# Optimization experiments

Measured on AMD Instinct MI355X. Metric: run time of the kernel, lower is better.

Reference implementation:

```python
import jax, jax.numpy as jnp
import numpy as np

EMBED_DIM = 1024
BOTTLENECK = 48          # adapter_hidden_dim (adapter_rank=0)
ADAPTER_WIDTH = 1        # multivector channels
MV_DIM = 16              # Cl(1,3) multivector dimension
N_GRADES = 5             # grades of sizes 1,4,6,4,1
LN_EPS = 1e-5

# grade projection mask [5,16]: grade0=idx0, grade1=1:5, grade2=5:11, grade3=11:15, grade4=15
_gm = np.zeros((N_GRADES, MV_DIM), dtype=np.float32)
_gm[0, 0] = 1.0
_gm[1, 1:5] = 1.0
_gm[2, 5:11] = 1.0
_gm[3, 11:15] = 1.0
_gm[4, 15] = 1.0
GRADE_MASK = jnp.asarray(_gm)


def setup_inputs() -> dict:
    key = jax.random.key(0)
    ks = jax.random.split(key, 8)
    B, N, D, R, W = 128, 256, EMBED_DIM, BOTTLENECK, ADAPTER_WIDTH
    x = jax.random.normal(ks[0], (B, N, D), dtype=jnp.float32)
    gamma = jnp.ones((D,), dtype=jnp.float32)
    beta = jnp.zeros((D,), dtype=jnp.float32)
    w_down = jax.random.normal(ks[1], (R, D), dtype=jnp.float32) / np.sqrt(D)
    w_to_mv = jax.random.normal(ks[2], (W * MV_DIM, R), dtype=jnp.float32) / np.sqrt(R)
    w_equi = jax.random.normal(ks[3], (W, W, N_GRADES), dtype=jnp.float32)
    b_equi = jnp.zeros((W,), dtype=jnp.float32)
    w_from_mv = jax.random.normal(ks[4], (R, W * MV_DIM), dtype=jnp.float32) / np.sqrt(W * MV_DIM)
    w_up = jax.random.normal(ks[5], (D, R), dtype=jnp.float32) / np.sqrt(R)
    scale = jnp.float32(0.001)
    return {"x": x, "gamma": gamma, "beta": beta, "w_down": w_down,
            "w_to_mv": w_to_mv, "w_equi": w_equi, "b_equi": b_equi,
            "w_from_mv": w_from_mv, "w_up": w_up, "scale": scale}


def reference(x, gamma, beta, w_down, w_to_mv, w_equi, b_equi, w_from_mv, w_up, scale):
    B, N, D = x.shape
    # LayerNorm
    mu = jnp.mean(x, axis=-1, keepdims=True)
    var = jnp.mean(jnp.square(x - mu), axis=-1, keepdims=True)
    h = (x - mu) * jax.lax.rsqrt(var + LN_EPS) * gamma + beta
    # down + GELU (exact, matching torch F.gelu default)
    h = jax.nn.gelu(jnp.einsum('bnd,rd->bnr', h, w_down), approximate=False)
    # to multivectors [B,N,C,16]
    mv = jnp.einsum('bnr,mr->bnm', h, w_to_mv).reshape(B, N, -1, MV_DIM)
    # EquiLinear: per-grade channel mixing + scalar bias
    mv = jnp.einsum('oik,kj,bnij->bnoj', w_equi, GRADE_MASK, mv)
    mv = mv.at[..., 0].add(b_equi)
    # from multivectors + GELU
    h = jax.nn.gelu(jnp.einsum('bnm,rm->bnr', mv.reshape(B, N, -1), w_from_mv),
                    approximate=False)
    # up (dropout p=0 is identity) and scaled residual
    h = jnp.einsum('bnr,dr->bnd', h, w_up)
    return x + scale * h
```

## Files before the change

kernel.cpp:

```cpp
#include <hip/hip_runtime.h>
#include <hip/hip_bf16.h>


typedef __attribute__((ext_vector_type(8))) short short8;
typedef __attribute__((ext_vector_type(4))) short short4b;
typedef __attribute__((ext_vector_type(4))) float float4a;

#define NTOK 32768
#define D 1024

__device__ __forceinline__ short f2bf(float x) {
    unsigned u = __float_as_uint(x);
    unsigned r = u + 0x7FFFu + ((u >> 16) & 1u);
    return (short)(r >> 16);
}
__device__ __forceinline__ float bf2f(short s) {
    return __uint_as_float(((unsigned)(unsigned short)s) << 16);
}
__device__ __forceinline__ float gelu_exact(float v) {
    return 0.5f * v * (1.0f + erff(v * 0.70710678118654752f));
}

__global__ void prep_weights(const float* __restrict__ wdn_f, const float* __restrict__ wup_f,
                             const float* __restrict__ gamma, const float* __restrict__ beta,
                             short* __restrict__ wdn_b, short* __restrict__ wup_b,
                             float* __restrict__ c12) {
    int blk = blockIdx.x;
    int tid = threadIdx.x;
    if (blk < 192) {
        int o = blk * 256 + tid;
        int j = o & 7, lane = (o >> 3) & 63, kt = (o >> 9) & 31, cb = o >> 14;
        int r = cb * 16 + (lane & 15);
        int d = kt * 32 + (lane >> 4) * 8 + j;
        wdn_b[o] = f2bf(wdn_f[r * 1024 + d] * gamma[d]);
    } else if (blk < 448) {
        int o2 = (blk - 192) * 256 + tid;
        int j = o2 & 7, lane = (o2 >> 3) & 63, kt = (o2 >> 9) & 1, cb = o2 >> 10;
        int dcol = cb * 16 + (lane & 15);
        int r = kt * 32 + (lane >> 4) * 8 + j;
        wup_b[o2] = (r < 48) ? f2bf(wup_f[dcol * 48 + r]) : (short)0;
    } else {
        int r = blk - 448;
        float a = 0.f, b = 0.f;
#pragma unroll
        for (int i = 0; i < 4; ++i) {
            int d = tid + 256 * i;
            float wv = wdn_f[r * 1024 + d];
            a = fmaf(wv, gamma[d], a);
            b = fmaf(wv, beta[d], b);
        }
#pragma unroll
        for (int off = 32; off; off >>= 1) {
            a += __shfl_xor(a, off);
            b += __shfl_xor(b, off);
        }
        __shared__ float red[8];
        int lane = tid & 63, w = tid >> 6;
        if (lane == 0) { red[w] = a; red[4 + w] = b; }
        __syncthreads();
        if (tid == 0) {
            c12[r]      = red[0] + red[1] + red[2] + red[3];
            c12[48 + r] = red[4] + red[5] + red[6] + red[7];
        }
    }
}

__launch_bounds__(256, 4)
__global__ void adapter_main(const float* __restrict__ x, const float* __restrict__ w_to_mv,
                             const float* __restrict__ w_equi, const float* __restrict__ b_equi,
                             const float* __restrict__ w_from_mv, const float* __restrict__ scale_p,
                             const short* __restrict__ wdn_b, const short* __restrict__ wup_b,
                             const float* __restrict__ c12, float* __restrict__ out) {
    __shared__ __align__(16) short xsh[16][1032];
    __shared__ __align__(16) float scratch[1568];
    short* zbuf = (short*)scratch;

    const int tid  = threadIdx.x;
    const int lane = tid & 63;
    const int w    = tid >> 6;
    const int q    = lane >> 4;
    const int m    = lane & 15;
    const long token0 = (long)blockIdx.x * 16;

    {
        const float4* xr = (const float4*)(x + token0 * D);
        float4 v[16];
#pragma unroll
        for (int t = 0; t < 4; ++t)
#pragma unroll
            for (int i = 0; i < 4; ++i)
                v[t * 4 + i] = xr[(w * 4 + t) * 256 + lane + 64 * i];

#pragma unroll
        for (int t = 0; t < 4; ++t) {
            int tok = w * 4 + t;
            float s1 = 0.f, s2 = 0.f;
#pragma unroll
            for (int i = 0; i < 4; ++i) {
                float4 vv = v[t * 4 + i];
                s1 += vv.x + vv.y + vv.z + vv.w;
                s2 += vv.x * vv.x + vv.y * vv.y + vv.z * vv.z + vv.w * vv.w;
            }
#pragma unroll
            for (int off = 32; off; off >>= 1) {
                s1 += __shfl_xor(s1, off);
                s2 += __shfl_xor(s2, off);
            }
            float mu  = s1 * (1.0f / 1024.0f);
            float var = fmaf(-mu, mu, s2 * (1.0f / 1024.0f));
            float rs  = rsqrtf(var + 1e-5f);
#pragma unroll
            for (int i = 0; i < 4; ++i) {
                int d0 = 4 * lane + 256 * i;
                float4 vv = v[t * 4 + i];
                short4b xs = {f2bf(vv.x), f2bf(vv.y), f2bf(vv.z), f2bf(vv.w)};
                *(short4b*)&xsh[tok][d0] = xs;
            }
            if (lane == 0) {
                scratch[1536 + tok] = rs;
                scratch[1552 + tok] = -mu * rs;
            }
        }
    }
    __syncthreads();

#pragma unroll
    for (int rep = 0; rep < 2; ++rep) {
        int jid = w + rep * 4;
        if (jid < 6) {
            int cb = jid % 3, kh = jid / 3;
            float4a acc = {0.f, 0.f, 0.f, 0.f};
            const short* bptr = wdn_b + ((cb * 32 + kh * 16) * 64 + lane) * 8;
            const short* aptr = &xsh[m][kh * 512 + q * 8];
#pragma unroll
            for (int kt = 0; kt < 16; ++kt) {
                short8 a = *(const short8*)(aptr + kt * 32);
                short8 b = *(const short8*)(bptr + kt * 512);
                acc = __builtin_amdgcn_mfma_f32_16x16x32_bf16(a, b, acc, 0, 0, 0);
            }
#pragma unroll
            for (int i = 0; i < 4; ++i)
                scratch[kh * 768 + (q * 4 + i) * 48 + cb * 16 + m] = acc[i];
        }
    }
    __syncthreads();

#pragma unroll
    for (int k = 0; k < 3; ++k) {
        int it = tid + k * 256;
        int tt = it / 48, r = it - tt * 48;
        float s = scratch[tt * 48 + r] + scratch[768 + tt * 48 + r];
        float y = fmaf(scratch[1536 + tt], s, fmaf(scratch[1552 + tt], c12[r], c12[48 + r]));
        scratch[tt * 48 + r] = gelu_exact(y);
    }
    __syncthreads();
    {
        int tt = tid >> 4, j = tid & 15;
        float acc = 0.f;
#pragma unroll 8
        for (int r = 0; r < 48; ++r) acc = fmaf(w_to_mv[j * 48 + r], scratch[tt * 48 + r], acc);
        int g = (j == 0) ? 0 : (j < 5) ? 1 : (j < 11) ? 2 : (j < 15) ? 3 : 4;
        acc *= w_equi[g];
        if (j == 0) acc += b_equi[0];
        scratch[768 + tt * 16 + j] = acc;
    }
    __syncthreads();
#pragma unroll
    for (int k = 0; k < 3; ++k) {
        int it = tid + k * 256;
        int tt = it / 48, r = it - tt * 48;
        float acc = 0.f;
#pragma unroll
        for (int j = 0; j < 16; ++j) acc = fmaf(w_from_mv[r * 16 + j], scratch[768 + tt * 16 + j], acc);
        float z = gelu_exact(acc);
        int kt = r >> 5, qq = (r >> 3) & 3, jj = r & 7;
        zbuf[kt * 512 + (qq * 16 + tt) * 8 + jj] = f2bf(z);
    }
    zbuf[768 + tid] = 0;
    __syncthreads();

    const float scale = scale_p[0];
    short8 a0 = *(const short8*)&zbuf[lane * 8];
    short8 a1 = *(const short8*)&zbuf[512 + lane * 8];
    long rowbase = (token0 + q * 4) * D;
#pragma unroll 4
    for (int cc = 0; cc < 16; ++cc) {
        int cb = w * 16 + cc;
        short8 b0 = *(const short8*)(wup_b + (cb * 2 + 0) * 512 + lane * 8);
        short8 b1 = *(const short8*)(wup_b + (cb * 2 + 1) * 512 + lane * 8);
        float4a acc = {0.f, 0.f, 0.f, 0.f};
        acc = __builtin_amdgcn_mfma_f32_16x16x32_bf16(a0, b0, acc, 0, 0, 0);
        acc = __builtin_amdgcn_mfma_f32_16x16x32_bf16(a1, b1, acc, 0, 0, 0);
        int d = cb * 16 + m;
#pragma unroll
        for (int i = 0; i < 4; ++i) {
            int tok = q * 4 + i;
            float xv = bf2f(xsh[tok][d]);
            out[rowbase + (long)i * D + d] = fmaf(scale, acc[i], xv);
        }
    }
}

extern "C" void kernel_launch(void* const* d_in, const int* in_sizes, int n_in,
                              void* d_out, int out_size, void* d_ws, size_t ws_size,
                              hipStream_t stream) {
    const float* x         = (const float*)d_in[0];
    const float* gamma     = (const float*)d_in[1];
    const float* beta      = (const float*)d_in[2];
    const float* w_down    = (const float*)d_in[3];
    const float* w_to_mv   = (const float*)d_in[4];
    const float* w_equi    = (const float*)d_in[5];
    const float* b_equi    = (const float*)d_in[6];
    const float* w_from_mv = (const float*)d_in[7];
    const float* w_up      = (const float*)d_in[8];
    const float* scale_p   = (const float*)d_in[9];

    short* wdn_b = (short*)d_ws;
    short* wup_b = wdn_b + 49152;
    float* c12   = (float*)(wup_b + 65536);

    prep_weights<<<496, 256, 0, stream>>>(w_down, w_up, gamma, beta, wdn_b, wup_b, c12);
    adapter_main<<<NTOK / 16, 256, 0, stream>>>(
        x, w_to_mv, w_equi, b_equi, w_from_mv, scale_p,
        wdn_b, wup_b, c12, (float*)d_out);
}
```

Measured before the change: 262.3 us.

## Process two 16-token chunks per block and prefetch the second chunk's x

Each block now handles 32 tokens as two 16-token chunks and issues the global loads for the second chunk before computing the first, so load latency can overlap the MFMA and epilogue work. It also replaces __syncthreads with a custom LDS-only barrier that waits only on lgkmcnt, so outstanding global loads are not drained. The grid halves to 1024 blocks. The cost is 16 extra float4 registers per thread under a launch bound of 4 blocks per CU, which may cause spills, and fewer blocks to spread across the CUs.

Result: slower. 283.4 us (+8.0%).

```diff
diff --git a/kernel.cpp b/kernel.cpp
--- a/kernel.cpp
+++ b/kernel.cpp
@@ -8,6 +8,7 @@
 
 #define NTOK 32768
 #define D 1024
+#define NBLK 1024
 
 __device__ __forceinline__ short f2bf(float x) {
     unsigned u = __float_as_uint(x);
@@ -19,6 +20,12 @@
 }
 __device__ __forceinline__ float gelu_exact(float v) {
     return 0.5f * v * (1.0f + erff(v * 0.70710678118654752f));
+}
+
+__device__ __forceinline__ void bar_lds() {
+    asm volatile("s_waitcnt lgkmcnt(0)" ::: "memory");
+    __builtin_amdgcn_s_barrier();
+    asm volatile("" ::: "memory");
 }
 
 __global__ void prep_weights(const float* __restrict__ wdn_f, const float* __restrict__ wup_f,
@@ -80,16 +87,20 @@
     const int w    = tid >> 6;
     const int q    = lane >> 4;
     const int m    = lane & 15;
-    const long token0 = (long)blockIdx.x * 16;
-
-    {
-        const float4* xr = (const float4*)(x + token0 * D);
-        float4 v[16];
-#pragma unroll
-        for (int t = 0; t < 4; ++t)
-#pragma unroll
-            for (int i = 0; i < 4; ++i)
-                v[t * 4 + i] = xr[(w * 4 + t) * 256 + lane + 64 * i];
+    const long tokbase = (long)blockIdx.x * 32;
+    const float scale = scale_p[0];
+
+    const float4* xr = (const float4*)(x + tokbase * D);
+    float4 v[16];
+#pragma unroll
+    for (int t = 0; t < 4; ++t)
+#pragma unroll
+        for (int i = 0; i < 4; ++i)
+            v[t * 4 + i] = xr[(w * 4 + t) * 256 + lane + 64 * i];
+
+#pragma unroll
+    for (int c = 0; c < 2; ++c) {
+        const long token0 = tokbase + c * 16;
 
 #pragma unroll
         for (int t = 0; t < 4; ++t) {
@@ -121,82 +132,97 @@
                 scratch[1552 + tok] = -mu * rs;
             }
         }
-    }
-    __syncthreads();
-
-#pragma unroll
-    for (int rep = 0; rep < 2; ++rep) {
-        int jid = w + rep * 4;
-        if (jid < 6) {
-            int cb = jid % 3, kh = jid / 3;
+
+        float4 vn[16];
+        if (c == 0) {
+            const float4* xr2 = (const float4*)(x + (tokbase + 16) * D);
+#pragma unroll
+            for (int t = 0; t < 4; ++t)
+#pragma unroll
+                for (int i = 0; i < 4; ++i)
+                    vn[t * 4 + i] = xr2[(w * 4 + t) * 256 + lane + 64 * i];
+        }
+        bar_lds();
+
+#pragma unroll
+        for (int rep = 0; rep < 2; ++rep) {
+            int jid = w + rep * 4;
+            if (jid < 6) {
+                int cb = jid % 3, kh = jid / 3;
+                float4a acc = {0.f, 0.f, 0.f, 0.f};
+                const short* bptr = wdn_b + ((cb * 32 + kh * 16) * 64 + lane) * 8;
+                const short* aptr = &xsh[m][kh * 512 + q * 8];
+#pragma unroll
+                for (int kt = 0; kt < 16; ++kt) {
+                    short8 a = *(const short8*)(aptr + kt * 32);
+                    short8 b = *(const short8*)(bptr + kt * 512);
+                    acc = __builtin_amdgcn_mfma_f32_16x16x32_bf16(a, b, acc, 0, 0, 0);
+                }
+#pragma unroll
+                for (int i = 0; i < 4; ++i)
+                    scratch[kh * 768 + (q * 4 + i) * 48 + cb * 16 + m] = acc[i];
+            }
+        }
+        bar_lds();
+
+#pragma unroll
+        for (int k = 0; k < 3; ++k) {
+            int it = tid + k * 256;
+            int tt = it / 48, r = it - tt * 48;
+            float s = scratch[tt * 48 + r] + scratch[768 + tt * 48 + r];
+            float y = fmaf(scratch[1536 + tt], s, fmaf(scratch[1552 + tt], c12[r], c12[48 + r]));
+            scratch[tt * 48 + r] = gelu_exact(y);
+        }
+        bar_lds();
+        {
+            int tt = tid >> 4, j = tid & 15;
+            float acc = 0.f;
+#pragma unroll 8
+            for (int r = 0; r < 48; ++r) acc = fmaf(w_to_mv[j * 48 + r], scratch[tt * 48 + r], acc);
+            int g = (j == 0) ? 0 : (j < 5) ? 1 : (j < 11) ? 2 : (j < 15) ? 3 : 4;
+            acc *= w_equi[g];
+            if (j == 0) acc += b_equi[0];
+            scratch[768 + tt * 16 + j] = acc;
+        }
+        bar_lds();
+#pragma unroll
+        for (int k = 0; k < 3; ++k) {
+            int it = tid + k * 256;
+            int tt = it / 48, r = it - tt * 48;
+            float acc = 0.f;
+#pragma unroll
+            for (int j = 0; j < 16; ++j) acc = fmaf(w_from_mv[r * 16 + j], scratch[768 + tt * 16 + j], acc);
+            float z = gelu_exact(acc);
+            int kt = r >> 5, qq = (r >> 3) & 3, jj = r & 7;
+            zbuf[kt * 512 + (qq * 16 + tt) * 8 + jj] = f2bf(z);
+        }
+        zbuf[768 + tid] = 0;
+        bar_lds();
+
+        short8 a0 = *(const short8*)&zbuf[lane * 8];
+        short8 a1 = *(const short8*)&zbuf[512 + lane * 8];
+        long rowbase = (token0 + q * 4) * D;
+#pragma unroll 4
+        for (int cc = 0; cc < 16; ++cc) {
+            int cb = w * 16 + cc;
+            short8 b0 = *(const short8*)(wup_b + (cb * 2 + 0) * 512 + lane * 8);
+            short8 b1 = *(const short8*)(wup_b + (cb * 2 + 1) * 512 + lane * 8);
             float4a acc = {0.f, 0.f, 0.f, 0.f};
-            const short* bptr = wdn_b + ((cb * 32 + kh * 16) * 64 + lane) * 8;
-            const short* aptr = &xsh[m][kh * 512 + q * 8];
-#pragma unroll
-            for (int kt = 0; kt < 16; ++kt) {
-                short8 a = *(const short8*)(aptr + kt * 32);
-                short8 b = *(const short8*)(bptr + kt * 512);
-                acc = __builtin_amdgcn_mfma_f32_16x16x32_bf16(a, b, acc, 0, 0, 0);
-            }
-#pragma unroll
-            for (int i = 0; i < 4; ++i)
-                scratch[kh * 768 + (q * 4 + i) * 48 + cb * 16 + m] = acc[i];
-        }
-    }
-    __syncthreads();
-
-#pragma unroll
-    for (int k = 0; k < 3; ++k) {
-        int it = tid + k * 256;
-        int tt = it / 48, r = it - tt * 48;
-        float s = scratch[tt * 48 + r] + scratch[768 + tt * 48 + r];
-        float y = fmaf(scratch[1536 + tt], s, fmaf(scratch[1552 + tt], c12[r], c12[48 + r]));
-        scratch[tt * 48 + r] = gelu_exact(y);
-    }
-    __syncthreads();
-    {
-        int tt = tid >> 4, j = tid & 15;
-        float acc = 0.f;
-#pragma unroll 8
-        for (int r = 0; r < 48; ++r) acc = fmaf(w_to_mv[j * 48 + r], scratch[tt * 48 + r], acc);
-        int g = (j == 0) ? 0 : (j < 5) ? 1 : (j < 11) ? 2 : (j < 15) ? 3 : 4;
-        acc *= w_equi[g];
-        if (j == 0) acc += b_equi[0];
-        scratch[768 + tt * 16 + j] = acc;
-    }
-    __syncthreads();
-#pragma unroll
-    for (int k = 0; k < 3; ++k) {
-        int it = tid + k * 256;
-        int tt = it / 48, r = it - tt * 48;
-        float acc = 0.f;
-#pragma unroll
-        for (int j = 0; j < 16; ++j) acc = fmaf(w_from_mv[r * 16 + j], scratch[768 + tt * 16 + j], acc);
-        float z = gelu_exact(acc);
-        int kt = r >> 5, qq = (r >> 3) & 3, jj = r & 7;
-        zbuf[kt * 512 + (qq * 16 + tt) * 8 + jj] = f2bf(z);
-    }
-    zbuf[768 + tid] = 0;
-    __syncthreads();
-
-    const float scale = scale_p[0];
-    short8 a0 = *(const short8*)&zbuf[lane * 8];
-    short8 a1 = *(const short8*)&zbuf[512 + lane * 8];
-    long rowbase = (token0 + q * 4) * D;
-#pragma unroll 4
-    for (int cc = 0; cc < 16; ++cc) {
-        int cb = w * 16 + cc;
-        short8 b0 = *(const short8*)(wup_b + (cb * 2 + 0) * 512 + lane * 8);
-        short8 b1 = *(const short8*)(wup_b + (cb * 2 + 1) * 512 + lane * 8);
-        float4a acc = {0.f, 0.f, 0.f, 0.f};
-        acc = __builtin_amdgcn_mfma_f32_16x16x32_bf16(a0, b0, acc, 0, 0, 0);
-        acc = __builtin_amdgcn_mfma_f32_16x16x32_bf16(a1, b1, acc, 0, 0, 0);
-        int d = cb * 16 + m;
-#pragma unroll
-        for (int i = 0; i < 4; ++i) {
-            int tok = q * 4 + i;
-            float xv = bf2f(xsh[tok][d]);
-            out[rowbase + (long)i * D + d] = fmaf(scale, acc[i], xv);
+            acc = __builtin_amdgcn_mfma_f32_16x16x32_bf16(a0, b0, acc, 0, 0, 0);
+            acc = __builtin_amdgcn_mfma_f32_16x16x32_bf16(a1, b1, acc, 0, 0, 0);
+            int d = cb * 16 + m;
+#pragma unroll
+            for (int i = 0; i < 4; ++i) {
+                int tok = q * 4 + i;
+                float xv = bf2f(xsh[tok][d]);
+                out[rowbase + (long)i * D + d] = fmaf(scale, acc[i], xv);
+            }
+        }
+
+        if (c == 0) {
+            bar_lds();
+#pragma unroll
+            for (int i2 = 0; i2 < 16; ++i2) v[i2] = vn[i2];
         }
     }
 }
@@ -220,7 +246,7 @@
     float* c12   = (float*)(wup_b + 65536);
 
     prep_weights<<<496, 256, 0, stream>>>(w_down, w_up, gamma, beta, wdn_b, wup_b, c12);
-    adapter_main<<<NTOK / 16, 256, 0, stream>>>(
+    adapter_main<<<NBLK, 256, 0, stream>>>(
         x, w_to_mv, w_equi, b_equi, w_from_mv, scale_p,
         wdn_b, wup_b, c12, (float*)d_out);
 }
```

## Process 32 tokens per 512-thread block, reusing weight fragments across two token tiles

Applied to the files above, without the earlier changes.

Doubles the tokens per block to 32 and the threads to 512, so each block handles two 16-token M-tiles. The down-projection now has six waves, each doing a full-K MFMA chain over one (tile, column-block) pair, which removes the split-K partial sums. The up-projection prefetches its w_up fragments into registers before the barrier and reuses each one for both token tiles, halving weight traffic per token. Barriers become a raw s_barrier after an LDS waitcnt. The costs are a larger LDS footprint and higher register pressure, which may lower occupancy, and two waves sit idle during the down-projection.

Result: no change. 264.5 us (+0.8%).

```diff
diff --git a/kernel.cpp b/kernel.cpp
--- a/kernel.cpp
+++ b/kernel.cpp
@@ -8,6 +8,8 @@
 
 #define NTOK 32768
 #define D 1024
+#define TOK 32
+#define NBLK (NTOK / TOK)
 
 __device__ __forceinline__ short f2bf(float x) {
     unsigned u = __float_as_uint(x);
@@ -19,6 +21,12 @@
 }
 __device__ __forceinline__ float gelu_exact(float v) {
     return 0.5f * v * (1.0f + erff(v * 0.70710678118654752f));
+}
+
+__device__ __forceinline__ void bar_lds() {
+    asm volatile("s_waitcnt lgkmcnt(0)" ::: "memory");
+    __builtin_amdgcn_s_barrier();
+    asm volatile("" ::: "memory");
 }
 
 __global__ void prep_weights(const float* __restrict__ wdn_f, const float* __restrict__ wup_f,
@@ -65,14 +73,14 @@
     }
 }
 
-__launch_bounds__(256, 4)
+__launch_bounds__(512, 4)
 __global__ void adapter_main(const float* __restrict__ x, const float* __restrict__ w_to_mv,
                              const float* __restrict__ w_equi, const float* __restrict__ b_equi,
                              const float* __restrict__ w_from_mv, const float* __restrict__ scale_p,
                              const short* __restrict__ wdn_b, const short* __restrict__ wup_b,
                              const float* __restrict__ c12, float* __restrict__ out) {
-    __shared__ __align__(16) short xsh[16][1032];
-    __shared__ __align__(16) float scratch[1568];
+    __shared__ __align__(16) short xsh[TOK][1032];
+    __shared__ __align__(16) float scratch[2112];
     short* zbuf = (short*)scratch;
 
     const int tid  = threadIdx.x;
@@ -80,7 +88,7 @@
     const int w    = tid >> 6;
     const int q    = lane >> 4;
     const int m    = lane & 15;
-    const long token0 = (long)blockIdx.x * 16;
+    const long token0 = (long)blockIdx.x * TOK;
 
     {
         const float4* xr = (const float4*)(x + token0 * D);
@@ -117,86 +125,94 @@
                 *(short4b*)&xsh[tok][d0] = xs;
             }
             if (lane == 0) {
-                scratch[1536 + tok] = rs;
-                scratch[1552 + tok] = -mu * rs;
-            }
-        }
-    }
-    __syncthreads();
-
-#pragma unroll
-    for (int rep = 0; rep < 2; ++rep) {
-        int jid = w + rep * 4;
-        if (jid < 6) {
-            int cb = jid % 3, kh = jid / 3;
-            float4a acc = {0.f, 0.f, 0.f, 0.f};
-            const short* bptr = wdn_b + ((cb * 32 + kh * 16) * 64 + lane) * 8;
-            const short* aptr = &xsh[m][kh * 512 + q * 8];
-#pragma unroll
-            for (int kt = 0; kt < 16; ++kt) {
-                short8 a = *(const short8*)(aptr + kt * 32);
-                short8 b = *(const short8*)(bptr + kt * 512);
-                acc = __builtin_amdgcn_mfma_f32_16x16x32_bf16(a, b, acc, 0, 0, 0);
-            }
-#pragma unroll
-            for (int i = 0; i < 4; ++i)
-                scratch[kh * 768 + (q * 4 + i) * 48 + cb * 16 + m] = acc[i];
-        }
-    }
-    __syncthreads();
+                scratch[2048 + tok] = rs;
+                scratch[2080 + tok] = -mu * rs;
+            }
+        }
+    }
+    bar_lds();
+
+    if (w < 6) {
+        int mt = w & 1, cb = w >> 1;
+        float4a acc = {0.f, 0.f, 0.f, 0.f};
+        const short* bptr = wdn_b + cb * 16384 + lane * 8;
+        const short* aptr = &xsh[mt * 16 + m][q * 8];
+#pragma unroll
+        for (int kt = 0; kt < 32; ++kt) {
+            short8 a = *(const short8*)(aptr + kt * 32);
+            short8 b = *(const short8*)(bptr + kt * 512);
+            acc = __builtin_amdgcn_mfma_f32_16x16x32_bf16(a, b, acc, 0, 0, 0);
+        }
+#pragma unroll
+        for (int i = 0; i < 4; ++i)
+            scratch[(mt * 16 + q * 4 + i) * 48 + cb * 16 + m] = acc[i];
+    }
+    bar_lds();
 
 #pragma unroll
     for (int k = 0; k < 3; ++k) {
-        int it = tid + k * 256;
+        int it = tid + k * 512;
         int tt = it / 48, r = it - tt * 48;
-        float s = scratch[tt * 48 + r] + scratch[768 + tt * 48 + r];
-        float y = fmaf(scratch[1536 + tt], s, fmaf(scratch[1552 + tt], c12[r], c12[48 + r]));
-        scratch[tt * 48 + r] = gelu_exact(y);
-    }
-    __syncthreads();
+        float y = fmaf(scratch[2048 + tt], scratch[it],
+                       fmaf(scratch[2080 + tt], c12[r], c12[48 + r]));
+        scratch[it] = gelu_exact(y);
+    }
+    bar_lds();
     {
         int tt = tid >> 4, j = tid & 15;
         float acc = 0.f;
-#pragma unroll 8
+#pragma unroll
         for (int r = 0; r < 48; ++r) acc = fmaf(w_to_mv[j * 48 + r], scratch[tt * 48 + r], acc);
         int g = (j == 0) ? 0 : (j < 5) ? 1 : (j < 11) ? 2 : (j < 15) ? 3 : 4;
         acc *= w_equi[g];
         if (j == 0) acc += b_equi[0];
-        scratch[768 + tt * 16 + j] = acc;
-    }
-    __syncthreads();
+        scratch[1536 + tt * 16 + j] = acc;
+    }
+    bar_lds();
 #pragma unroll
     for (int k = 0; k < 3; ++k) {
-        int it = tid + k * 256;
+        int it = tid + k * 512;
         int tt = it / 48, r = it - tt * 48;
         float acc = 0.f;
 #pragma unroll
-        for (int j = 0; j < 16; ++j) acc = fmaf(w_from_mv[r * 16 + j], scratch[768 + tt * 16 + j], acc);
+        for (int j = 0; j < 16; ++j)
+            acc = fmaf(w_from_mv[r * 16 + j], scratch[1536 + tt * 16 + j], acc);
         float z = gelu_exact(acc);
+        int mt = tt >> 4, ttl = tt & 15;
         int kt = r >> 5, qq = (r >> 3) & 3, jj = r & 7;
-        zbuf[kt * 512 + (qq * 16 + tt) * 8 + jj] = f2bf(z);
-    }
-    zbuf[768 + tid] = 0;
-    __syncthreads();
+        zbuf[mt * 1024 + kt * 512 + (qq * 16 + ttl) * 8 + jj] = f2bf(z);
+    }
+    zbuf[(tid >> 8) * 1024 + 768 + (tid & 255)] = 0;
+
+    short8 b0[8], b1[8];
+#pragma unroll
+    for (int c = 0; c < 8; ++c) {
+        int cb = w * 8 + c;
+        b0[c] = *(const short8*)(wup_b + (cb * 2 + 0) * 512 + lane * 8);
+        b1[c] = *(const short8*)(wup_b + (cb * 2 + 1) * 512 + lane * 8);
+    }
+    bar_lds();
 
     const float scale = scale_p[0];
-    short8 a0 = *(const short8*)&zbuf[lane * 8];
-    short8 a1 = *(const short8*)&zbuf[512 + lane * 8];
-    long rowbase = (token0 + q * 4) * D;
-#pragma unroll 4
-    for (int cc = 0; cc < 16; ++cc) {
-        int cb = w * 16 + cc;
-        short8 b0 = *(const short8*)(wup_b + (cb * 2 + 0) * 512 + lane * 8);
-        short8 b1 = *(const short8*)(wup_b + (cb * 2 + 1) * 512 + lane * 8);
-        float4a acc = {0.f, 0.f, 0.f, 0.f};
-        acc = __builtin_amdgcn_mfma_f32_16x16x32_bf16(a0, b0, acc, 0, 0, 0);
-        acc = __builtin_amdgcn_mfma_f32_16x16x32_bf16(a1, b1, acc, 0, 0, 0);
+    short8 a00 = *(const short8*)&zbuf[           lane * 8];
+    short8 a01 = *(const short8*)&zbuf[ 512 +     lane * 8];
+    short8 a10 = *(const short8*)&zbuf[1024 +     lane * 8];
+    short8 a11 = *(const short8*)&zbuf[1536 +     lane * 8];
+#pragma unroll
+    for (int c = 0; c < 8; ++c) {
+        int cb = w * 8 + c;
         int d = cb * 16 + m;
+        float4a acc0 = {0.f, 0.f, 0.f, 0.f};
+        acc0 = __builtin_amdgcn_mfma_f32_16x16x32_bf16(a00, b0[c], acc0, 0, 0, 0);
+        acc0 = __builtin_amdgcn_mfma_f32_16x16x32_bf16(a01, b1[c], acc0, 0, 0, 0);
+        float4a acc1 = {0.f, 0.f, 0.f, 0.f};
+        acc1 = __builtin_amdgcn_mfma_f32_16x16x32_bf16(a10, b0[c], acc1, 0, 0, 0);
+        acc1 = __builtin_amdgcn_mfma_f32_16x16x32_bf16(a11, b1[c], acc1, 0, 0, 0);
 #pragma unroll
         for (int i = 0; i < 4; ++i) {
-            int tok = q * 4 + i;
-            float xv = bf2f(xsh[tok][d]);
-            out[rowbase + (long)i * D + d] = fmaf(scale, acc[i], xv);
+            int t0 = q * 4 + i;
+            out[(token0 + t0) * D + d]      = fmaf(scale, acc0[i], bf2f(xsh[t0][d]));
+            out[(token0 + 16 + t0) * D + d] = fmaf(scale, acc1[i], bf2f(xsh[16 + t0][d]));
         }
     }
 }
@@ -220,7 +236,7 @@
     float* c12   = (float*)(wup_b + 65536);
 
     prep_weights<<<496, 256, 0, stream>>>(w_down, w_up, gamma, beta, wdn_b, wup_b, c12);
-    adapter_main<<<NTOK / 16, 256, 0, stream>>>(
+    adapter_main<<<NBLK, 512, 0, stream>>>(
         x, w_to_mv, w_equi, b_equi, w_from_mv, scale_p,
         wdn_b, wup_b, c12, (float*)d_out);
 }
```
